# Performance work log

Hardware: AMD Instinct MI355X
Metric: run time of the kernel (lower is better)

## Reference

```python
import jax, jax.numpy as jnp
import numpy as np

LAMBDA_COLOR = 10.0


def _neighbors(x, p):
    """Patch-unfold: x [B,C,H,W] -> [B, P*P, C, H, W] of zero-padded shifted copies.
    Matches conv3d with diagonal one-hot [P^2,1,1,P,P] weights, padding (0,pad,pad)."""
    pad = (p - 1) // 2
    B, C, H, W = x.shape
    xp = jnp.pad(x, ((0, 0), (0, 0), (pad, pad), (pad, pad)))
    shifts = [xp[:, :, i:i + H, j:j + W] for i in range(p) for j in range(p)]
    return jnp.stack(shifts, axis=1)


def _spatial_grid(img_size):
    # np.mgrid[-1:1+eps:2/(S-1), -1:1+eps:2/(S-1)] -> [2, S, S] (y-coords, x-coords)
    lin = jnp.linspace(-1.0, 1.0, img_size, dtype=jnp.float32)
    gy, gx = jnp.meshgrid(lin, lin, indexing='ij')
    return jnp.stack([gy, gx], axis=0)[None]  # [1, 2, S, S]


def setup_inputs() -> dict:
    key = jax.random.key(0)
    k1, k2 = jax.random.split(key)
    B, S, P = 16, 256, 7
    flow = jax.random.normal(k1, (B, 2, S, S), dtype=jnp.float32)
    image = jax.random.uniform(k2, (B, 3, S, S), dtype=jnp.float32)
    return {"flow": flow, "image": image, "img_size": S, "patch_size": P}


def reference(flow, image, img_size, patch_size):
    flow = flow * img_size                                  # [B,2,H,W]
    grid = _spatial_grid(img_size)                          # [1,2,H,W]

    flow_nb = _neighbors(flow, patch_size)                  # [B,P2,2,H,W]
    img_nb = _neighbors(image, patch_size)                  # [B,P2,3,H,W]
    grid_nb = _neighbors(grid, patch_size)                  # [1,P2,2,H,W]

    im_w = jnp.sum((image[:, None] - img_nb) ** 2, axis=2)  # [B,P2,H,W]
    sp_w = jnp.sum((grid[:, None] - grid_nb) ** 2, axis=2)  # [1,P2,H,W]
    fl = jnp.sum((flow_nb - flow[:, None]) ** 2, axis=2)    # [B,P2,H,W]

    return jnp.mean(fl * jnp.exp(-(im_w * LAMBDA_COLOR + sp_w)))
```

## Files before the change

kernel.cpp:

```cpp
#include <hip/hip_runtime.h>


#define S_DIM 256
#define PAD 3
#define TILE_X 64
#define TILE_Y 16
#define CX 4
#define QX (TILE_X / CX)
#define HALO_X (TILE_X + 2*PAD)
#define HALO_Y (TILE_Y + 2*PAD)
#define LSTRIDE 72
#define N_TERMS 51380224.0f

__global__ void init_out_kernel(float* out) { out[0] = 0.0f; }

__global__ __launch_bounds__(256) void flow_reg_loss_kernel(
    const float* __restrict__ flow,
    const float* __restrict__ image,
    float* __restrict__ out)
{
    __shared__ float sm[5][HALO_Y][LSTRIDE];
    __shared__ float wave_sums[4];

    const int b   = blockIdx.z;
    const int tx0 = blockIdx.x * TILE_X;
    const int ty0 = blockIdx.y * TILE_Y;
    const int tid = threadIdx.y * QX + threadIdx.x;

    const float* img_b = image + (size_t)b * 3 * S_DIM * S_DIM;
    const float* flw_b = flow  + (size_t)b * 2 * S_DIM * S_DIM;

    for (int e = tid; e < HALO_Y * HALO_X; e += 256) {
        const int ly = e / HALO_X;
        const int lx = e - ly * HALO_X;
        const int gy = ty0 - PAD + ly;
        const int gx = tx0 - PAD + lx;
        float i0 = 0.f, i1 = 0.f, i2 = 0.f, f0 = 0.f, f1 = 0.f;
        if ((unsigned)gy < S_DIM && (unsigned)gx < S_DIM) {
            const int g = gy * S_DIM + gx;
            i0 = img_b[0 * S_DIM * S_DIM + g];
            i1 = img_b[1 * S_DIM * S_DIM + g];
            i2 = img_b[2 * S_DIM * S_DIM + g];
            f0 = flw_b[0 * S_DIM * S_DIM + g] * 256.0f;
            f1 = flw_b[1 * S_DIM * S_DIM + g] * 256.0f;
        }
        sm[0][ly][lx] = i0;
        sm[1][ly][lx] = i1;
        sm[2][ly][lx] = i2;
        sm[3][ly][lx] = f0;
        sm[4][ly][lx] = f1;
    }
    __syncthreads();

    const int qx = threadIdx.x;
    const int ty = threadIdx.y;
    const int cy = ty + PAD;
    const int xb = qx * CX;
    const int y  = ty0 + ty;
    const int x0 = tx0 + xb;

    float ic0[CX], ic1[CX], ic2[CX], fc0[CX], fc1[CX];
#pragma unroll
    for (int i = 0; i < CX; ++i) {
        ic0[i] = sm[0][cy][xb + PAD + i];
        ic1[i] = sm[1][cy][xb + PAD + i];
        ic2[i] = sm[2][cy][xb + PAD + i];
        fc0[i] = sm[3][cy][xb + PAD + i];
        fc1[i] = sm[4][cy][xb + PAD + i];
    }

    const float step = 2.0f / 255.0f;
    const float K2 = step * step;
    const float gyc = -1.0f + step * (float)y;
    float g2c[CX];
#pragma unroll
    for (int i = 0; i < CX; ++i) {
        const float gxc = -1.0f + step * (float)(x0 + i);
        g2c[i] = gyc * gyc + gxc * gxc;
    }

    float acc[CX] = {0.f, 0.f, 0.f, 0.f};

#pragma unroll
    for (int dy = -PAD; dy <= PAD; ++dy) {
        const int ny = cy + dy;
        const bool yin = (unsigned)(y + dy) < S_DIM;

        float r[5][12];
#pragma unroll
        for (int c = 0; c < 5; ++c) {
            const float4 a  = *(const float4*)&sm[c][ny][xb];
            const float4 b4 = *(const float4*)&sm[c][ny][xb + 4];
            const float4 c4 = *(const float4*)&sm[c][ny][xb + 8];
            r[c][0] = a.x;  r[c][1] = a.y;  r[c][2]  = a.z;  r[c][3]  = a.w;
            r[c][4] = b4.x; r[c][5] = b4.y; r[c][6]  = b4.z; r[c][7]  = b4.w;
            r[c][8] = c4.x; r[c][9] = c4.y; r[c][10] = c4.z; r[c][11] = c4.w;
        }

#pragma unroll
        for (int dx = -PAD; dx <= PAD; ++dx) {
            const float spw_in = K2 * (float)(dy * dy + dx * dx);
#pragma unroll
            for (int i = 0; i < CX; ++i) {
                const int j = i + dx + PAD;
                const float d0 = ic0[i] - r[0][j];
                const float d1 = ic1[i] - r[1][j];
                const float d2 = ic2[i] - r[2][j];
                const float imw = d0 * d0 + d1 * d1 + d2 * d2;
                const float e0 = r[3][j] - fc0[i];
                const float e1 = r[4][j] - fc1[i];
                const float fl2 = e0 * e0 + e1 * e1;
                const bool inb = yin && ((unsigned)(x0 + i + dx) < S_DIM);
                const float spw = inb ? spw_in : g2c[i];
                acc[i] += fl2 * __expf(-(imw * 10.0f + spw));
            }
        }
    }

    float acc_all = (acc[0] + acc[1]) + (acc[2] + acc[3]);
#pragma unroll
    for (int off = 32; off > 0; off >>= 1)
        acc_all += __shfl_down(acc_all, off, 64);
    if ((tid & 63) == 0) wave_sums[tid >> 6] = acc_all;
    __syncthreads();
    if (tid == 0) {
        const float s = wave_sums[0] + wave_sums[1] + wave_sums[2] + wave_sums[3];
        atomicAdd(out, s * (1.0f / N_TERMS));
    }
}

extern "C" void kernel_launch(void* const* d_in, const int* in_sizes, int n_in,
                              void* d_out, int out_size, void* d_ws, size_t ws_size,
                              hipStream_t stream) {
    const float* flow  = (const float*)d_in[0];
    const float* image = (const float*)d_in[1];
    float* out = (float*)d_out;

    init_out_kernel<<<1, 1, 0, stream>>>(out);

    dim3 grid(S_DIM / TILE_X, S_DIM / TILE_Y, 16);
    dim3 block(QX, TILE_Y);
    flow_reg_loss_kernel<<<grid, block, 0, stream>>>(flow, image, out);
}
```

Before: 97.57 us.

## Exploit pair symmetry to halve neighbor evaluations and handle padding analytically

The weighted term is symmetric in each pixel-neighbor pair, so the kernel now sums only half the stencil offsets (forward row offsets plus the positive-dx half of the center row) and doubles the result. Zero-padded out-of-bounds neighbors all give the same value, so they are counted and added in closed form per pixel. The halo shrinks to the lower rows only, which cuts shared-memory loads and exp evaluations roughly in half. The cost is more involved boundary-count logic and a change in floating-point summation order.

```diff
diff --git a/kernel.cpp b/kernel.cpp
--- a/kernel.cpp
+++ b/kernel.cpp
@@ -8,7 +8,7 @@
 #define CX 4
 #define QX (TILE_X / CX)
 #define HALO_X (TILE_X + 2*PAD)
-#define HALO_Y (TILE_Y + 2*PAD)
+#define HALO_Y (TILE_Y + PAD)
 #define LSTRIDE 72
 #define N_TERMS 51380224.0f
 
@@ -33,7 +33,7 @@
     for (int e = tid; e < HALO_Y * HALO_X; e += 256) {
         const int ly = e / HALO_X;
         const int lx = e - ly * HALO_X;
-        const int gy = ty0 - PAD + ly;
+        const int gy = ty0 + ly;
         const int gx = tx0 - PAD + lx;
         float i0 = 0.f, i1 = 0.f, i2 = 0.f, f0 = 0.f, f1 = 0.f;
         if ((unsigned)gy < S_DIM && (unsigned)gx < S_DIM) {
@@ -54,38 +54,55 @@
 
     const int qx = threadIdx.x;
     const int ty = threadIdx.y;
-    const int cy = ty + PAD;
     const int xb = qx * CX;
     const int y  = ty0 + ty;
     const int x0 = tx0 + xb;
 
+    const float step = 2.0f / 255.0f;
+    const float K2 = step * step;
+
+    float acc = 0.0f;
     float ic0[CX], ic1[CX], ic2[CX], fc0[CX], fc1[CX];
+
+    {
+        float r[5][12];
 #pragma unroll
-    for (int i = 0; i < CX; ++i) {
-        ic0[i] = sm[0][cy][xb + PAD + i];
-        ic1[i] = sm[1][cy][xb + PAD + i];
-        ic2[i] = sm[2][cy][xb + PAD + i];
-        fc0[i] = sm[3][cy][xb + PAD + i];
-        fc1[i] = sm[4][cy][xb + PAD + i];
+        for (int c = 0; c < 5; ++c) {
+            const float4 a  = *(const float4*)&sm[c][ty][xb];
+            const float4 b4 = *(const float4*)&sm[c][ty][xb + 4];
+            const float4 c4 = *(const float4*)&sm[c][ty][xb + 8];
+            r[c][0] = a.x;  r[c][1] = a.y;  r[c][2]  = a.z;  r[c][3]  = a.w;
+            r[c][4] = b4.x; r[c][5] = b4.y; r[c][6]  = b4.z; r[c][7]  = b4.w;
+            r[c][8] = c4.x; r[c][9] = c4.y; r[c][10] = c4.z; r[c][11] = c4.w;
+        }
+#pragma unroll
+        for (int i = 0; i < CX; ++i) {
+            ic0[i] = r[0][3 + i]; ic1[i] = r[1][3 + i]; ic2[i] = r[2][3 + i];
+            fc0[i] = r[3][3 + i]; fc1[i] = r[4][3 + i];
+        }
+#pragma unroll
+        for (int dx = 1; dx <= PAD; ++dx) {
+            const float spw_in = K2 * (float)(dx * dx);
+#pragma unroll
+            for (int i = 0; i < CX; ++i) {
+                const int j = i + dx + 3;
+                const float d0 = ic0[i] - r[0][j];
+                const float d1 = ic1[i] - r[1][j];
+                const float d2 = ic2[i] - r[2][j];
+                const float imw = d0 * d0 + d1 * d1 + d2 * d2;
+                const float e0 = r[3][j] - fc0[i];
+                const float e1 = r[4][j] - fc1[i];
+                const float fl2 = e0 * e0 + e1 * e1;
+                const float w = ((unsigned)(x0 + i + dx) < S_DIM) ? 1.0f : 0.0f;
+                acc += (w * fl2) * __expf(-(imw * 10.0f + spw_in));
+            }
+        }
     }
 
-    const float step = 2.0f / 255.0f;
-    const float K2 = step * step;
-    const float gyc = -1.0f + step * (float)y;
-    float g2c[CX];
 #pragma unroll
-    for (int i = 0; i < CX; ++i) {
-        const float gxc = -1.0f + step * (float)(x0 + i);
-        g2c[i] = gyc * gyc + gxc * gxc;
-    }
-
-    float acc[CX] = {0.f, 0.f, 0.f, 0.f};
-
-#pragma unroll
-    for (int dy = -PAD; dy <= PAD; ++dy) {
-        const int ny = cy + dy;
-        const bool yin = (unsigned)(y + dy) < S_DIM;
-
+    for (int dy = 1; dy <= PAD; ++dy) {
+        const int ny = ty + dy;
+        const bool yin = (y + dy) < S_DIM;
         float r[5][12];
 #pragma unroll
         for (int c = 0; c < 5; ++c) {
@@ -96,13 +113,12 @@
             r[c][4] = b4.x; r[c][5] = b4.y; r[c][6]  = b4.z; r[c][7]  = b4.w;
             r[c][8] = c4.x; r[c][9] = c4.y; r[c][10] = c4.z; r[c][11] = c4.w;
         }
-
 #pragma unroll
         for (int dx = -PAD; dx <= PAD; ++dx) {
             const float spw_in = K2 * (float)(dy * dy + dx * dx);
 #pragma unroll
             for (int i = 0; i < CX; ++i) {
-                const int j = i + dx + PAD;
+                const int j = i + dx + 3;
                 const float d0 = ic0[i] - r[0][j];
                 const float d1 = ic1[i] - r[1][j];
                 const float d2 = ic2[i] - r[2][j];
@@ -110,14 +126,28 @@
                 const float e0 = r[3][j] - fc0[i];
                 const float e1 = r[4][j] - fc1[i];
                 const float fl2 = e0 * e0 + e1 * e1;
-                const bool inb = yin && ((unsigned)(x0 + i + dx) < S_DIM);
-                const float spw = inb ? spw_in : g2c[i];
-                acc[i] += fl2 * __expf(-(imw * 10.0f + spw));
+                const float w = (yin && (unsigned)(x0 + i + dx) < S_DIM) ? 1.0f : 0.0f;
+                acc += (w * fl2) * __expf(-(imw * 10.0f + spw_in));
             }
         }
     }
 
-    float acc_all = (acc[0] + acc[1]) + (acc[2] + acc[3]);
+    const int ny_in = 7 - max(0, 3 - y) - max(0, y - (S_DIM - 1 - 3));
+    const float gyc = -1.0f + step * (float)y;
+    float oob = 0.0f;
+#pragma unroll
+    for (int i = 0; i < CX; ++i) {
+        const int xg = x0 + i;
+        const int nx_in = 7 - max(0, 3 - xg) - max(0, xg - (S_DIM - 1 - 3));
+        const float n_oob = (float)(49 - ny_in * nx_in);
+        const float gxc = -1.0f + step * (float)xg;
+        const float g2c = gyc * gyc + gxc * gxc;
+        const float imw_c = ic0[i] * ic0[i] + ic1[i] * ic1[i] + ic2[i] * ic2[i];
+        const float fl_c  = fc0[i] * fc0[i] + fc1[i] * fc1[i];
+        oob += (n_oob * fl_c) * __expf(-(imw_c * 10.0f + g2c));
+    }
+
+    float acc_all = 2.0f * acc + oob;
 #pragma unroll
     for (int off = 32; off > 0; off >>= 1)
         acc_all += __shfl_down(acc_all, off, 64);
```

Result: faster. 91.15 us (-6.6%).
